# Performance work log

Hardware: AMD Instinct MI355X
Metric: run time of the kernel (lower is better)

Reference implementation:

```python
import jax, jax.numpy as jnp
import numpy as np

B = 65536          # graphs (agents)
NODES_PER = 9      # 1 torso + 8 joints
N = B * NODES_PER
D = 64
SOFTPLUS_BIAS = float(np.log(np.expm1(1.0)))  # biased_softplus_1.0 from NormalParamExtractor


def _star_edges():
    # bidirectional torso<->joint star per 9-node graph
    base = np.arange(B, dtype=np.int64) * NODES_PER          # torso ids [B]
    torso = np.repeat(base, 8)                               # [8B]
    joint = (base[:, None] + np.arange(1, 9, dtype=np.int64)[None, :]).reshape(-1)  # [8B]
    src = np.concatenate([torso, joint])                     # torso->joint, joint->torso
    dst = np.concatenate([joint, torso])
    return jnp.asarray(np.stack([src, dst], axis=0))         # [2, 16B]


def setup_inputs() -> dict:
    key = jax.random.key(0)
    ks = jax.random.split(key, 12)
    s = lambda fan_in: 1.0 / np.sqrt(fan_in)
    inp = {
        "x": jax.random.normal(ks[0], (N, 11), dtype=jnp.float32),
        "edge_index": _star_edges(),
        # input projections
        "W_joint": jax.random.uniform(ks[1], (2, D), jnp.float32, -s(2), s(2)),
        "b_joint": jnp.zeros((D,), jnp.float32),
        "W_torso": jax.random.uniform(ks[2], (11, D), jnp.float32, -s(11), s(11)),
        "b_torso": jnp.zeros((D,), jnp.float32),
        # GraphConv 1: lin_rel (bias) on aggregated neighbors + lin_root (no bias)
        "W_rel1": jax.random.uniform(ks[3], (D, D), jnp.float32, -s(D), s(D)),
        "b_rel1": jnp.zeros((D,), jnp.float32),
        "W_root1": jax.random.uniform(ks[4], (D, D), jnp.float32, -s(D), s(D)),
        # GraphConv 2
        "W_rel2": jax.random.uniform(ks[5], (D, D), jnp.float32, -s(D), s(D)),
        "b_rel2": jnp.zeros((D,), jnp.float32),
        "W_root2": jax.random.uniform(ks[6], (D, D), jnp.float32, -s(D), s(D)),
        # 8 per-joint heads Linear(64, 2)
        "W_heads": jax.random.uniform(ks[7], (8, D, 2), jnp.float32, -s(D), s(D)),
        "b_heads": jnp.zeros((8, 2), jnp.float32),
    }
    return inp


def _graph_conv(h, src, dst, W_rel, b_rel, W_root, n):
    # GraphConv (aggr='add'): out[i] = lin_rel(sum_{j->i} h[j]) + lin_root(h[i])
    agg = jax.ops.segment_sum(h[src], dst, num_segments=n)   # [N, D]
    return agg @ W_rel + b_rel + h @ W_root


def reference(x, edge_index, W_joint, b_joint, W_torso, b_torso,
              W_rel1, b_rel1, W_root1, W_rel2, b_rel2, W_root2,
              W_heads, b_heads):
    n = x.shape[0]
    b = n // NODES_PER
    xg = x.reshape(b, NODES_PER, 11)
    h_torso = xg[:, :1, :] @ W_torso + b_torso              # [b, 1, D]  (node 0 of each graph)
    h_joint = xg[:, 1:, :2] @ W_joint + b_joint             # [b, 8, D]
    h = jnp.concatenate([h_torso, h_joint], axis=1).reshape(n, D)
    src, dst = edge_index[0], edge_index[1]
    h = jnp.tanh(_graph_conv(h, src, dst, W_rel1, b_rel1, W_root1, n))
    h = jnp.tanh(_graph_conv(h, src, dst, W_rel2, b_rel2, W_root2, n))
    joints = h.reshape(b, NODES_PER, D)[:, 1:, :]           # [b, 8, D]
    out = jnp.einsum('bjd,jdo->bjo', joints, W_heads) + b_heads  # [b, 8, 2]
    loc = out[..., 0]                                       # [b, 8]
    scale = jax.nn.softplus(out[..., 1] + SOFTPLUS_BIAS)    # biased_softplus_1.0
    return loc, scale
```

## Files before the change

kernel.cpp:

```cpp
#include <hip/hip_runtime.h>


typedef __attribute__((ext_vector_type(8))) short bf16x8;
typedef __attribute__((ext_vector_type(4))) float f32x4;

#define SOFTPLUS_BIAS 0.5413248546129181f

#define LDS_H   0
#define LDS_S   18432
#define LDS_SZ  20480

__device__ __forceinline__ unsigned int cvtpk(float lo, float hi) {
  unsigned int r;
  asm("v_cvt_pk_bf16_f32 %0, %1, %2" : "=v"(r) : "v"(lo), "v"(hi));
  return r;
}
__device__ __forceinline__ float asf(unsigned int u) {
  union { unsigned int i; float f; } v; v.i = u; return v.f;
}
__device__ __forceinline__ unsigned short f2bf(float f) {
  union { float f; unsigned int i; } v; v.f = f;
  unsigned int lsb = (v.i >> 16) & 1u;
  return (unsigned short)((v.i + 0x7fffu + lsb) >> 16);
}
__device__ __forceinline__ float fast_tanh(float x) {
  float e = __expf(2.0f * x);
  return 1.0f - 2.0f * __builtin_amdgcn_rcpf(e + 1.0f);
}

__global__ void pack_weights(const float* __restrict__ Wrel1, const float* __restrict__ Wroot1,
                             const float* __restrict__ Wrel2, const float* __restrict__ Wroot2,
                             const float* __restrict__ Wheads, unsigned short* __restrict__ ws) {
  int id = blockIdx.x * 256 + threadIdx.x;
  if (id < 16384) {
    const float* W = (id < 4096) ? Wrel1 : (id < 8192) ? Wroot1 : (id < 12288) ? Wrel2 : Wroot2;
    int m = id & 4095;
    int e = m & 7, lane = (m >> 3) & 63, nt = (m >> 9) & 3, ks = m >> 11;
    int k = ((lane >> 4) << 3) + e + (ks << 5);
    int col = (nt << 4) + (lane & 15);
    ws[id] = f2bf(W[k * 64 + col]);
  } else if (id < 17408) {
    int m = id - 16384;
    int e = m & 7, lane = (m >> 3) & 63, ks = m >> 9;
    int k = ((lane >> 4) << 3) + e + (ks << 5);
    int c = lane & 15, j = c >> 1, o = c & 1;
    ws[id] = f2bf(Wheads[(j * 64 + k) * 2 + o]);
  }
}

__launch_bounds__(256, 5)
__global__ void actor_main(const float* __restrict__ x,
                           const float* __restrict__ Wj_g, const float* __restrict__ bj_g,
                           const float* __restrict__ Wt_g, const float* __restrict__ bt_g,
                           const float* __restrict__ brel1_g, const float* __restrict__ brel2_g,
                           const float* __restrict__ bh_g,
                           const unsigned short* __restrict__ wsw,
                           float* __restrict__ out) {
  __shared__ __align__(16) unsigned char smem[LDS_SZ];
  const int t = threadIdx.x;
  const int lane = t & 63;
  const int w = t >> 6;
  const int gbase = blockIdx.x << 4;
  const int l15 = lane & 15;
  const int q = lane >> 4;
  const int ks16 = q << 4;
  const int relc = l15 + (w << 4);

  const bf16x8* wsv = reinterpret_cast<const bf16x8*>(wsw);

  bf16x8 bRel0  = wsv[(0 + w) * 64 + lane];
  bf16x8 bRel1  = wsv[(4 + w) * 64 + lane];
  bf16x8 bRoot0 = wsv[512 + (0 + w) * 64 + lane];
  bf16x8 bRoot1 = wsv[512 + (4 + w) * 64 + lane];

  float Wtr[11];
#pragma unroll
  for (int k = 0; k < 11; k++) Wtr[k] = Wt_g[k * 64 + lane];
  const float btr = bt_g[lane];
  const float Wj0 = Wj_g[lane], Wj1 = Wj_g[64 + lane], bjr = bj_g[lane];
  const float brelA = brel1_g[relc], brelB = brel2_g[relc];

  unsigned int aggA[9];
#pragma unroll
  for (int m = 0; m < 9; m++) {
    int r = (m << 4) + l15;
    int g = (57 * r) >> 9;
    int node = r - 9 * g;
    int row = (node == 0) ? g : 9 * g;
    unsigned int base = (node == 0) ? (unsigned)LDS_S : 0u;
    aggA[m] = base + row * 128 + (ks16 ^ ((row & 7) << 4));
  }
  const unsigned int h0b = l15 * 128 + (unsigned)(ks16 ^ ((l15 & 7) << 4));
  unsigned int wb[4];
#pragma unroll
  for (int i = 0; i < 4; i++) {
    int rr = (q << 2) + i;
    wb[i] = rr * 128 + (unsigned)((2 * relc) ^ ((rr & 7) << 4));
  }

  const int w_u = __builtin_amdgcn_readfirstlane(w);
#pragma unroll
  for (int it = 0; it < 4; it++) {
    const int g = w_u + (it << 2);
    const float* __restrict__ xr = x + (size_t)(gbase + g) * 99;
    float acc1 = btr;
#pragma unroll
    for (int k = 0; k < 11; k++) acc1 += xr[k] * Wtr[k];
    int trow = 9 * g;
    *reinterpret_cast<unsigned short*>(smem + trow * 128 + ((2 * lane) ^ ((trow & 7) << 4))) =
        (unsigned short)cvtpk(acc1, acc1);
    float sx0 = 0.f, sx1 = 0.f;
#pragma unroll
    for (int j = 0; j < 8; j++) {
      float x0 = xr[11 + 11 * j];
      float x1 = xr[12 + 11 * j];
      sx0 += x0; sx1 += x1;
      float accj = bjr + x0 * Wj0 + x1 * Wj1;
      int row = 9 * g + 1 + j;
      *reinterpret_cast<unsigned short*>(smem + row * 128 + ((2 * lane) ^ ((row & 7) << 4))) =
          (unsigned short)cvtpk(accj, accj);
    }
    float s = 8.0f * bjr + sx0 * Wj0 + sx1 * Wj1;
    *reinterpret_cast<unsigned short*>(smem + LDS_S + g * 128 + ((2 * lane) ^ ((g & 7) << 4))) =
        (unsigned short)cvtpk(s, s);
  }
  __syncthreads();

  f32x4 acc[9];
#pragma unroll
  for (int layer = 0; layer < 2; layer++) {
    const float brel = layer ? brelB : brelA;

    if (layer == 1) {
      bRel0  = wsv[1024 + (0 + w) * 64 + lane];
      bRel1  = wsv[1024 + (4 + w) * 64 + lane];
      bRoot0 = wsv[1024 + 512 + (0 + w) * 64 + lane];
      bRoot1 = wsv[1024 + 512 + (4 + w) * 64 + lane];
      int gS = t >> 4, dq = t & 15;
      int rb = dq << 3;
      float s0 = 0.f, s1 = 0.f, s2 = 0.f, s3 = 0.f;
#pragma unroll
      for (int j = 0; j < 8; j++) {
        int row = 9 * gS + 1 + j;
        uint2 p = *reinterpret_cast<const uint2*>(smem + row * 128 + (rb ^ ((row & 7) << 4)));
        s0 += asf(p.x << 16); s1 += asf(p.x & 0xffff0000u);
        s2 += asf(p.y << 16); s3 += asf(p.y & 0xffff0000u);
      }
      uint2 o; o.x = cvtpk(s0, s1); o.y = cvtpk(s2, s3);
      *reinterpret_cast<uint2*>(smem + LDS_S + gS * 128 + (rb ^ ((gS & 7) << 4))) = o;
      __syncthreads();
    }

#pragma unroll
    for (int m = 0; m < 9; m++) {
      bf16x8 ag0 = *reinterpret_cast<const bf16x8*>(smem + aggA[m]);
      bf16x8 ag1 = *reinterpret_cast<const bf16x8*>(smem + (aggA[m] ^ 64u));
      bf16x8 a0  = *reinterpret_cast<const bf16x8*>(smem + h0b + m * 2048);
      bf16x8 a1  = *reinterpret_cast<const bf16x8*>(smem + (h0b ^ 64u) + m * 2048);
      f32x4 c = {brel, brel, brel, brel};
      c = __builtin_amdgcn_mfma_f32_16x16x32_bf16(ag0, bRel0, c, 0, 0, 0);
      c = __builtin_amdgcn_mfma_f32_16x16x32_bf16(ag1, bRel1, c, 0, 0, 0);
      c = __builtin_amdgcn_mfma_f32_16x16x32_bf16(a0, bRoot0, c, 0, 0, 0);
      acc[m] = __builtin_amdgcn_mfma_f32_16x16x32_bf16(a1, bRoot1, c, 0, 0, 0);
    }
    __syncthreads();

#pragma unroll
    for (int m = 0; m < 9; m++) {
      const int off = m * 2048;
      unsigned p0 = cvtpk(fast_tanh(acc[m][0]), fast_tanh(acc[m][1]));
      unsigned p1 = cvtpk(fast_tanh(acc[m][2]), fast_tanh(acc[m][3]));
      *reinterpret_cast<unsigned short*>(smem + wb[0] + off) = (unsigned short)p0;
      *reinterpret_cast<unsigned short*>(smem + wb[1] + off) = (unsigned short)(p0 >> 16);
      *reinterpret_cast<unsigned short*>(smem + wb[2] + off) = (unsigned short)p1;
      *reinterpret_cast<unsigned short*>(smem + wb[3] + off) = (unsigned short)(p1 >> 16);
    }
    __syncthreads();
  }

  {
    bf16x8 hb0 = wsv[2048 + lane];
    bf16x8 hb1 = wsv[2048 + 64 + lane];
    int c = l15;
#pragma unroll
    for (int u = 0; u < 2; u++) {
      int tt = (w << 1) + u;
      int jr = (tt << 4) + l15;
      int arow = 9 * (jr >> 3) + 1 + (jr & 7);
      unsigned ha = arow * 128 + (unsigned)(ks16 ^ ((arow & 7) << 4));
      bf16x8 a0 = *reinterpret_cast<const bf16x8*>(smem + ha);
      bf16x8 a1 = *reinterpret_cast<const bf16x8*>(smem + (ha ^ 64u));
      f32x4 z = {0.f, 0.f, 0.f, 0.f};
      z = __builtin_amdgcn_mfma_f32_16x16x32_bf16(a0, hb0, z, 0, 0, 0);
      z = __builtin_amdgcn_mfma_f32_16x16x32_bf16(a1, hb1, z, 0, 0, 0);
#pragma unroll
      for (int i = 0; i < 4; i++) {
        int r = (tt << 4) + (q << 2) + i;
        int gg = r >> 3, j2 = r & 7;
        if (c == 2 * j2) {
          out[(size_t)(gbase + gg) * 8 + j2] = z[i] + bh_g[2 * j2];
        } else if (c == 2 * j2 + 1) {
          float zz = z[i] + bh_g[2 * j2 + 1] + SOFTPLUS_BIAS;
          float sp = (zz > 20.0f) ? zz : __logf(1.0f + __expf(zz));
          out[524288 + (size_t)(gbase + gg) * 8 + j2] = sp;
        }
      }
    }
  }
}

extern "C" void kernel_launch(void* const* d_in, const int* in_sizes, int n_in,
                              void* d_out, int out_size, void* d_ws, size_t ws_size,
                              hipStream_t stream) {
  const float* x      = (const float*)d_in[0];
  const float* Wj     = (const float*)d_in[2];
  const float* bj     = (const float*)d_in[3];
  const float* Wt     = (const float*)d_in[4];
  const float* bt     = (const float*)d_in[5];
  const float* Wrel1  = (const float*)d_in[6];
  const float* brel1  = (const float*)d_in[7];
  const float* Wroot1 = (const float*)d_in[8];
  const float* Wrel2  = (const float*)d_in[9];
  const float* brel2  = (const float*)d_in[10];
  const float* Wroot2 = (const float*)d_in[11];
  const float* Wheads = (const float*)d_in[12];
  const float* bh     = (const float*)d_in[13];
  unsigned short* ws16 = (unsigned short*)d_ws;
  float* out = (float*)d_out;

  hipLaunchKernelGGL(pack_weights, dim3(68), dim3(256), 0, stream,
                     Wrel1, Wroot1, Wrel2, Wroot2, Wheads, ws16);
  hipLaunchKernelGGL(actor_main, dim3(4096), dim3(256), 0, stream,
                     x, Wj, bj, Wt, bt, brel1, brel2, bh, ws16, out);
}
```

Before: 63.05 us.

## Split GraphConv MFMA tiles 2x2 across waves with padded 10-row graph layout

Each wave now handles half the row tiles and two column tiles, instead of all nine row tiles and one column tile. The A fragments loaded from LDS are reused across two output column tiles, which cuts LDS reads. Graphs are padded to 10 rows so the 160 rows split evenly into 5 tiles per wave half. This increases LDS size, lowers the launch-bound occupancy from 5 to 4, and adds 10% padding compute plus more weight registers.

```diff
diff --git a/kernel.cpp b/kernel.cpp
--- a/kernel.cpp
+++ b/kernel.cpp
@@ -6,9 +6,8 @@
 
 #define SOFTPLUS_BIAS 0.5413248546129181f
 
-#define LDS_H   0
-#define LDS_S   18432
-#define LDS_SZ  20480
+#define LDS_S   20480
+#define LDS_SZ  22528
 
 __device__ __forceinline__ unsigned int cvtpk(float lo, float hi) {
   unsigned int r;
@@ -48,7 +47,7 @@
   }
 }
 
-__launch_bounds__(256, 5)
+__launch_bounds__(256, 4)
 __global__ void actor_main(const float* __restrict__ x,
                            const float* __restrict__ Wj_g, const float* __restrict__ bj_g,
                            const float* __restrict__ Wt_g, const float* __restrict__ bt_g,
@@ -60,42 +59,43 @@
   const int t = threadIdx.x;
   const int lane = t & 63;
   const int w = t >> 6;
+  const int mh = w >> 1;
+  const int nh = w & 1;
   const int gbase = blockIdx.x << 4;
   const int l15 = lane & 15;
   const int q = lane >> 4;
   const int ks16 = q << 4;
-  const int relc = l15 + (w << 4);
+  const int relc0 = l15 + (nh << 5);
+  const int relc1 = relc0 + 16;
 
   const bf16x8* wsv = reinterpret_cast<const bf16x8*>(wsw);
-
-  bf16x8 bRel0  = wsv[(0 + w) * 64 + lane];
-  bf16x8 bRel1  = wsv[(4 + w) * 64 + lane];
-  bf16x8 bRoot0 = wsv[512 + (0 + w) * 64 + lane];
-  bf16x8 bRoot1 = wsv[512 + (4 + w) * 64 + lane];
 
   float Wtr[11];
 #pragma unroll
   for (int k = 0; k < 11; k++) Wtr[k] = Wt_g[k * 64 + lane];
   const float btr = bt_g[lane];
   const float Wj0 = Wj_g[lane], Wj1 = Wj_g[64 + lane], bjr = bj_g[lane];
-  const float brelA = brel1_g[relc], brelB = brel2_g[relc];
-
-  unsigned int aggA[9];
-#pragma unroll
-  for (int m = 0; m < 9; m++) {
-    int r = (m << 4) + l15;
-    int g = (57 * r) >> 9;
-    int node = r - 9 * g;
-    int row = (node == 0) ? g : 9 * g;
-    unsigned int base = (node == 0) ? (unsigned)LDS_S : 0u;
-    aggA[m] = base + row * 128 + (ks16 ^ ((row & 7) << 4));
-  }
-  const unsigned int h0b = l15 * 128 + (unsigned)(ks16 ^ ((l15 & 7) << 4));
-  unsigned int wb[4];
+  const float brelA0 = brel1_g[relc0], brelA1 = brel1_g[relc1];
+  const float brelB0 = brel2_g[relc0], brelB1 = brel2_g[relc1];
+
+  unsigned int aggA[5];
+#pragma unroll
+  for (int mm = 0; mm < 5; mm++) {
+    int r = ((5 * mh + mm) << 4) + l15;
+    int g = (r * 205) >> 11;
+    int node = r - 10 * g;
+    if (node == 0)
+      aggA[mm] = (unsigned)(LDS_S + g * 128 + (ks16 ^ ((g & 7) << 4)));
+    else
+      aggA[mm] = (unsigned)((10 * g) * 128 + (ks16 ^ (((10 * g) & 7) << 4)));
+  }
+  const unsigned int h0bW = l15 * 128 + (unsigned)(ks16 ^ ((l15 & 7) << 4)) + mh * 10240;
+  unsigned int wb0[4], wb1[4];
 #pragma unroll
   for (int i = 0; i < 4; i++) {
     int rr = (q << 2) + i;
-    wb[i] = rr * 128 + (unsigned)((2 * relc) ^ ((rr & 7) << 4));
+    wb0[i] = rr * 128 + (unsigned)((2 * relc0) ^ ((rr & 7) << 4)) + mh * 10240;
+    wb1[i] = rr * 128 + (unsigned)((2 * relc1) ^ ((rr & 7) << 4)) + mh * 10240;
   }
 
   const int w_u = __builtin_amdgcn_readfirstlane(w);
@@ -106,7 +106,7 @@
     float acc1 = btr;
 #pragma unroll
     for (int k = 0; k < 11; k++) acc1 += xr[k] * Wtr[k];
-    int trow = 9 * g;
+    int trow = 10 * g;
     *reinterpret_cast<unsigned short*>(smem + trow * 128 + ((2 * lane) ^ ((trow & 7) << 4))) =
         (unsigned short)cvtpk(acc1, acc1);
     float sx0 = 0.f, sx1 = 0.f;
@@ -116,7 +116,7 @@
       float x1 = xr[12 + 11 * j];
       sx0 += x0; sx1 += x1;
       float accj = bjr + x0 * Wj0 + x1 * Wj1;
-      int row = 9 * g + 1 + j;
+      int row = 10 * g + 1 + j;
       *reinterpret_cast<unsigned short*>(smem + row * 128 + ((2 * lane) ^ ((row & 7) << 4))) =
           (unsigned short)cvtpk(accj, accj);
     }
@@ -126,22 +126,29 @@
   }
   __syncthreads();
 
-  f32x4 acc[9];
+  const int nt0 = nh << 1;
+  f32x4 acc[5][2];
 #pragma unroll
   for (int layer = 0; layer < 2; layer++) {
-    const float brel = layer ? brelB : brelA;
+    const int lb = layer ? 1024 : 0;
+    bf16x8 bRel00  = wsv[lb + nt0 * 64 + lane];
+    bf16x8 bRel01  = wsv[lb + 256 + nt0 * 64 + lane];
+    bf16x8 bRel10  = wsv[lb + (nt0 + 1) * 64 + lane];
+    bf16x8 bRel11  = wsv[lb + 256 + (nt0 + 1) * 64 + lane];
+    bf16x8 bRoot00 = wsv[lb + 512 + nt0 * 64 + lane];
+    bf16x8 bRoot01 = wsv[lb + 768 + nt0 * 64 + lane];
+    bf16x8 bRoot10 = wsv[lb + 512 + (nt0 + 1) * 64 + lane];
+    bf16x8 bRoot11 = wsv[lb + 768 + (nt0 + 1) * 64 + lane];
+    const float brel0 = layer ? brelB0 : brelA0;
+    const float brel1 = layer ? brelB1 : brelA1;
 
     if (layer == 1) {
-      bRel0  = wsv[1024 + (0 + w) * 64 + lane];
-      bRel1  = wsv[1024 + (4 + w) * 64 + lane];
-      bRoot0 = wsv[1024 + 512 + (0 + w) * 64 + lane];
-      bRoot1 = wsv[1024 + 512 + (4 + w) * 64 + lane];
       int gS = t >> 4, dq = t & 15;
       int rb = dq << 3;
       float s0 = 0.f, s1 = 0.f, s2 = 0.f, s3 = 0.f;
 #pragma unroll
       for (int j = 0; j < 8; j++) {
-        int row = 9 * gS + 1 + j;
+        int row = 10 * gS + 1 + j;
         uint2 p = *reinterpret_cast<const uint2*>(smem + row * 128 + (rb ^ ((row & 7) << 4)));
         s0 += asf(p.x << 16); s1 += asf(p.x & 0xffff0000u);
         s2 += asf(p.y << 16); s3 += asf(p.y & 0xffff0000u);
@@ -152,28 +159,39 @@
     }
 
 #pragma unroll
-    for (int m = 0; m < 9; m++) {
-      bf16x8 ag0 = *reinterpret_cast<const bf16x8*>(smem + aggA[m]);
-      bf16x8 ag1 = *reinterpret_cast<const bf16x8*>(smem + (aggA[m] ^ 64u));
-      bf16x8 a0  = *reinterpret_cast<const bf16x8*>(smem + h0b + m * 2048);
-      bf16x8 a1  = *reinterpret_cast<const bf16x8*>(smem + (h0b ^ 64u) + m * 2048);
-      f32x4 c = {brel, brel, brel, brel};
-      c = __builtin_amdgcn_mfma_f32_16x16x32_bf16(ag0, bRel0, c, 0, 0, 0);
-      c = __builtin_amdgcn_mfma_f32_16x16x32_bf16(ag1, bRel1, c, 0, 0, 0);
-      c = __builtin_amdgcn_mfma_f32_16x16x32_bf16(a0, bRoot0, c, 0, 0, 0);
-      acc[m] = __builtin_amdgcn_mfma_f32_16x16x32_bf16(a1, bRoot1, c, 0, 0, 0);
+    for (int mm = 0; mm < 5; mm++) {
+      bf16x8 ag0 = *reinterpret_cast<const bf16x8*>(smem + aggA[mm]);
+      bf16x8 ag1 = *reinterpret_cast<const bf16x8*>(smem + (aggA[mm] ^ 64u));
+      bf16x8 a0  = *reinterpret_cast<const bf16x8*>(smem + h0bW + mm * 2048);
+      bf16x8 a1  = *reinterpret_cast<const bf16x8*>(smem + ((h0bW + mm * 2048) ^ 64u));
+      f32x4 c0 = {brel0, brel0, brel0, brel0};
+      c0 = __builtin_amdgcn_mfma_f32_16x16x32_bf16(ag0, bRel00, c0, 0, 0, 0);
+      c0 = __builtin_amdgcn_mfma_f32_16x16x32_bf16(ag1, bRel01, c0, 0, 0, 0);
+      c0 = __builtin_amdgcn_mfma_f32_16x16x32_bf16(a0, bRoot00, c0, 0, 0, 0);
+      acc[mm][0] = __builtin_amdgcn_mfma_f32_16x16x32_bf16(a1, bRoot01, c0, 0, 0, 0);
+      f32x4 c1 = {brel1, brel1, brel1, brel1};
+      c1 = __builtin_amdgcn_mfma_f32_16x16x32_bf16(ag0, bRel10, c1, 0, 0, 0);
+      c1 = __builtin_amdgcn_mfma_f32_16x16x32_bf16(ag1, bRel11, c1, 0, 0, 0);
+      c1 = __builtin_amdgcn_mfma_f32_16x16x32_bf16(a0, bRoot10, c1, 0, 0, 0);
+      acc[mm][1] = __builtin_amdgcn_mfma_f32_16x16x32_bf16(a1, bRoot11, c1, 0, 0, 0);
     }
     __syncthreads();
 
 #pragma unroll
-    for (int m = 0; m < 9; m++) {
-      const int off = m * 2048;
-      unsigned p0 = cvtpk(fast_tanh(acc[m][0]), fast_tanh(acc[m][1]));
-      unsigned p1 = cvtpk(fast_tanh(acc[m][2]), fast_tanh(acc[m][3]));
-      *reinterpret_cast<unsigned short*>(smem + wb[0] + off) = (unsigned short)p0;
-      *reinterpret_cast<unsigned short*>(smem + wb[1] + off) = (unsigned short)(p0 >> 16);
-      *reinterpret_cast<unsigned short*>(smem + wb[2] + off) = (unsigned short)p1;
-      *reinterpret_cast<unsigned short*>(smem + wb[3] + off) = (unsigned short)(p1 >> 16);
+    for (int mm = 0; mm < 5; mm++) {
+      const int off = mm * 2048;
+      unsigned p0 = cvtpk(fast_tanh(acc[mm][0][0]), fast_tanh(acc[mm][0][1]));
+      unsigned p1 = cvtpk(fast_tanh(acc[mm][0][2]), fast_tanh(acc[mm][0][3]));
+      *reinterpret_cast<unsigned short*>(smem + wb0[0] + off) = (unsigned short)p0;
+      *reinterpret_cast<unsigned short*>(smem + wb0[1] + off) = (unsigned short)(p0 >> 16);
+      *reinterpret_cast<unsigned short*>(smem + wb0[2] + off) = (unsigned short)p1;
+      *reinterpret_cast<unsigned short*>(smem + wb0[3] + off) = (unsigned short)(p1 >> 16);
+      unsigned p2 = cvtpk(fast_tanh(acc[mm][1][0]), fast_tanh(acc[mm][1][1]));
+      unsigned p3 = cvtpk(fast_tanh(acc[mm][1][2]), fast_tanh(acc[mm][1][3]));
+      *reinterpret_cast<unsigned short*>(smem + wb1[0] + off) = (unsigned short)p2;
+      *reinterpret_cast<unsigned short*>(smem + wb1[1] + off) = (unsigned short)(p2 >> 16);
+      *reinterpret_cast<unsigned short*>(smem + wb1[2] + off) = (unsigned short)p3;
+      *reinterpret_cast<unsigned short*>(smem + wb1[3] + off) = (unsigned short)(p3 >> 16);
     }
     __syncthreads();
   }
@@ -186,7 +204,7 @@
     for (int u = 0; u < 2; u++) {
       int tt = (w << 1) + u;
       int jr = (tt << 4) + l15;
-      int arow = 9 * (jr >> 3) + 1 + (jr & 7);
+      int arow = 10 * (jr >> 3) + 1 + (jr & 7);
       unsigned ha = arow * 128 + (unsigned)(ks16 ^ ((arow & 7) << 4));
       bf16x8 a0 = *reinterpret_cast<const bf16x8*>(smem + ha);
       bf16x8 a1 = *reinterpret_cast<const bf16x8*>(smem + (ha ^ 64u));
```

Result: slower. 70.13 us (+11.2%).

## Make each wave own four graphs to drop block-wide barriers

Applied to the files above, without the earlier changes.

Each wavefront now owns its own four graphs, kept in a private LDS region padded to 12 rows per graph. Each wave computes all 64 output columns over 3 M-tiles, so __syncthreads is replaced by compiler fences. Weights are reloaded per layer from global memory rather than held in registers. The per-wave accumulator grows to 12 tiles, so launch bounds drop from 5 to 3 blocks per CU, trading occupancy for removing cross-wave synchronisation. Padding to 12 rows also wastes a quarter of the MFMA rows.

```diff
diff --git a/kernel.cpp b/kernel.cpp
--- a/kernel.cpp
+++ b/kernel.cpp
@@ -5,10 +5,9 @@
 typedef __attribute__((ext_vector_type(4))) float f32x4;
 
 #define SOFTPLUS_BIAS 0.5413248546129181f
-
-#define LDS_H   0
-#define LDS_S   18432
-#define LDS_SZ  20480
+#define LDS_SB  24576
+#define LDS_SZ  26624
+#define FENCE() asm volatile("" ::: "memory")
 
 __device__ __forceinline__ unsigned int cvtpk(float lo, float hi) {
   unsigned int r;
@@ -48,7 +47,7 @@
   }
 }
 
-__launch_bounds__(256, 5)
+__launch_bounds__(256, 3)
 __global__ void actor_main(const float* __restrict__ x,
                            const float* __restrict__ Wj_g, const float* __restrict__ bj_g,
                            const float* __restrict__ Wt_g, const float* __restrict__ bt_g,
@@ -64,50 +63,45 @@
   const int l15 = lane & 15;
   const int q = lane >> 4;
   const int ks16 = q << 4;
-  const int relc = l15 + (w << 4);
+  const unsigned HB = (unsigned)(w * 6144);
+  const unsigned SB = (unsigned)(LDS_SB + w * 512);
 
   const bf16x8* wsv = reinterpret_cast<const bf16x8*>(wsw);
-
-  bf16x8 bRel0  = wsv[(0 + w) * 64 + lane];
-  bf16x8 bRel1  = wsv[(4 + w) * 64 + lane];
-  bf16x8 bRoot0 = wsv[512 + (0 + w) * 64 + lane];
-  bf16x8 bRoot1 = wsv[512 + (4 + w) * 64 + lane];
 
   float Wtr[11];
 #pragma unroll
   for (int k = 0; k < 11; k++) Wtr[k] = Wt_g[k * 64 + lane];
   const float btr = bt_g[lane];
   const float Wj0 = Wj_g[lane], Wj1 = Wj_g[64 + lane], bjr = bj_g[lane];
-  const float brelA = brel1_g[relc], brelB = brel2_g[relc];
-
-  unsigned int aggA[9];
-#pragma unroll
-  for (int m = 0; m < 9; m++) {
-    int r = (m << 4) + l15;
-    int g = (57 * r) >> 9;
-    int node = r - 9 * g;
-    int row = (node == 0) ? g : 9 * g;
-    unsigned int base = (node == 0) ? (unsigned)LDS_S : 0u;
-    aggA[m] = base + row * 128 + (ks16 ^ ((row & 7) << 4));
-  }
-  const unsigned int h0b = l15 * 128 + (unsigned)(ks16 ^ ((l15 & 7) << 4));
-  unsigned int wb[4];
-#pragma unroll
-  for (int i = 0; i < 4; i++) {
-    int rr = (q << 2) + i;
-    wb[i] = rr * 128 + (unsigned)((2 * relc) ^ ((rr & 7) << 4));
-  }
+  float brelA[4], brelB[4];
+#pragma unroll
+  for (int nt = 0; nt < 4; nt++) {
+    brelA[nt] = brel1_g[l15 + (nt << 4)];
+    brelB[nt] = brel2_g[l15 + (nt << 4)];
+  }
+
+  unsigned aggA[3];
+#pragma unroll
+  for (int mt = 0; mt < 3; mt++) {
+    int r = (mt << 4) + l15;
+    int g = (r * 43) >> 9;
+    int node = r - 12 * g;
+    int trow = 12 * g;
+    aggA[mt] = (node == 0)
+        ? (SB + g * 128 + (unsigned)(ks16 ^ (g << 4)))
+        : (HB + trow * 128 + (unsigned)(ks16 ^ ((trow & 7) << 4)));
+  }
+  const unsigned h0b = HB + l15 * 128 + (unsigned)(ks16 ^ ((l15 & 7) << 4));
 
   const int w_u = __builtin_amdgcn_readfirstlane(w);
 #pragma unroll
   for (int it = 0; it < 4; it++) {
-    const int g = w_u + (it << 2);
-    const float* __restrict__ xr = x + (size_t)(gbase + g) * 99;
+    const float* __restrict__ xr = x + (size_t)(gbase + (w_u << 2) + it) * 99;
     float acc1 = btr;
 #pragma unroll
     for (int k = 0; k < 11; k++) acc1 += xr[k] * Wtr[k];
-    int trow = 9 * g;
-    *reinterpret_cast<unsigned short*>(smem + trow * 128 + ((2 * lane) ^ ((trow & 7) << 4))) =
+    int trow = 12 * it;
+    *reinterpret_cast<unsigned short*>(smem + HB + trow * 128 + ((2 * lane) ^ ((trow & 7) << 4))) =
         (unsigned short)cvtpk(acc1, acc1);
     float sx0 = 0.f, sx1 = 0.f;
 #pragma unroll
@@ -116,78 +110,100 @@
       float x1 = xr[12 + 11 * j];
       sx0 += x0; sx1 += x1;
       float accj = bjr + x0 * Wj0 + x1 * Wj1;
-      int row = 9 * g + 1 + j;
-      *reinterpret_cast<unsigned short*>(smem + row * 128 + ((2 * lane) ^ ((row & 7) << 4))) =
+      int row = 12 * it + 1 + j;
+      *reinterpret_cast<unsigned short*>(smem + HB + row * 128 + ((2 * lane) ^ ((row & 7) << 4))) =
           (unsigned short)cvtpk(accj, accj);
     }
     float s = 8.0f * bjr + sx0 * Wj0 + sx1 * Wj1;
-    *reinterpret_cast<unsigned short*>(smem + LDS_S + g * 128 + ((2 * lane) ^ ((g & 7) << 4))) =
+    *reinterpret_cast<unsigned short*>(smem + SB + it * 128 + ((2 * lane) ^ (it << 4))) =
         (unsigned short)cvtpk(s, s);
   }
-  __syncthreads();
-
-  f32x4 acc[9];
+  FENCE();
+
+  f32x4 acc[3][4];
 #pragma unroll
   for (int layer = 0; layer < 2; layer++) {
-    const float brel = layer ? brelB : brelA;
+    const int lb = layer ? 1024 : 0;
 
     if (layer == 1) {
-      bRel0  = wsv[1024 + (0 + w) * 64 + lane];
-      bRel1  = wsv[1024 + (4 + w) * 64 + lane];
-      bRoot0 = wsv[1024 + 512 + (0 + w) * 64 + lane];
-      bRoot1 = wsv[1024 + 512 + (4 + w) * 64 + lane];
-      int gS = t >> 4, dq = t & 15;
+      int gS = lane >> 4, dq = lane & 15;
       int rb = dq << 3;
       float s0 = 0.f, s1 = 0.f, s2 = 0.f, s3 = 0.f;
 #pragma unroll
       for (int j = 0; j < 8; j++) {
-        int row = 9 * gS + 1 + j;
-        uint2 p = *reinterpret_cast<const uint2*>(smem + row * 128 + (rb ^ ((row & 7) << 4)));
+        int row = 12 * gS + 1 + j;
+        uint2 p = *reinterpret_cast<const uint2*>(smem + HB + row * 128 + (rb ^ ((row & 7) << 4)));
         s0 += asf(p.x << 16); s1 += asf(p.x & 0xffff0000u);
         s2 += asf(p.y << 16); s3 += asf(p.y & 0xffff0000u);
       }
       uint2 o; o.x = cvtpk(s0, s1); o.y = cvtpk(s2, s3);
-      *reinterpret_cast<uint2*>(smem + LDS_S + gS * 128 + (rb ^ ((gS & 7) << 4))) = o;
-      __syncthreads();
-    }
-
-#pragma unroll
-    for (int m = 0; m < 9; m++) {
-      bf16x8 ag0 = *reinterpret_cast<const bf16x8*>(smem + aggA[m]);
-      bf16x8 ag1 = *reinterpret_cast<const bf16x8*>(smem + (aggA[m] ^ 64u));
-      bf16x8 a0  = *reinterpret_cast<const bf16x8*>(smem + h0b + m * 2048);
-      bf16x8 a1  = *reinterpret_cast<const bf16x8*>(smem + (h0b ^ 64u) + m * 2048);
-      f32x4 c = {brel, brel, brel, brel};
-      c = __builtin_amdgcn_mfma_f32_16x16x32_bf16(ag0, bRel0, c, 0, 0, 0);
-      c = __builtin_amdgcn_mfma_f32_16x16x32_bf16(ag1, bRel1, c, 0, 0, 0);
-      c = __builtin_amdgcn_mfma_f32_16x16x32_bf16(a0, bRoot0, c, 0, 0, 0);
-      acc[m] = __builtin_amdgcn_mfma_f32_16x16x32_bf16(a1, bRoot1, c, 0, 0, 0);
-    }
-    __syncthreads();
-
-#pragma unroll
-    for (int m = 0; m < 9; m++) {
-      const int off = m * 2048;
-      unsigned p0 = cvtpk(fast_tanh(acc[m][0]), fast_tanh(acc[m][1]));
-      unsigned p1 = cvtpk(fast_tanh(acc[m][2]), fast_tanh(acc[m][3]));
-      *reinterpret_cast<unsigned short*>(smem + wb[0] + off) = (unsigned short)p0;
-      *reinterpret_cast<unsigned short*>(smem + wb[1] + off) = (unsigned short)(p0 >> 16);
-      *reinterpret_cast<unsigned short*>(smem + wb[2] + off) = (unsigned short)p1;
-      *reinterpret_cast<unsigned short*>(smem + wb[3] + off) = (unsigned short)(p1 >> 16);
-    }
-    __syncthreads();
+      *reinterpret_cast<uint2*>(smem + SB + gS * 128 + (rb ^ (gS << 4))) = o;
+      FENCE();
+    }
+
+    bf16x8 bf[4][2];
+#pragma unroll
+    for (int nt = 0; nt < 4; nt++) {
+      bf[nt][0] = wsv[lb + nt * 64 + lane];
+      bf[nt][1] = wsv[lb + 256 + nt * 64 + lane];
+    }
+#pragma unroll
+    for (int mt = 0; mt < 3; mt++) {
+      bf16x8 ag0 = *reinterpret_cast<const bf16x8*>(smem + aggA[mt]);
+      bf16x8 ag1 = *reinterpret_cast<const bf16x8*>(smem + (aggA[mt] ^ 64u));
+#pragma unroll
+      for (int nt = 0; nt < 4; nt++) {
+        float br = layer ? brelB[nt] : brelA[nt];
+        f32x4 c = {br, br, br, br};
+        c = __builtin_amdgcn_mfma_f32_16x16x32_bf16(ag0, bf[nt][0], c, 0, 0, 0);
+        acc[mt][nt] = __builtin_amdgcn_mfma_f32_16x16x32_bf16(ag1, bf[nt][1], c, 0, 0, 0);
+      }
+    }
+#pragma unroll
+    for (int nt = 0; nt < 4; nt++) {
+      bf[nt][0] = wsv[lb + 512 + nt * 64 + lane];
+      bf[nt][1] = wsv[lb + 768 + nt * 64 + lane];
+    }
+#pragma unroll
+    for (int mt = 0; mt < 3; mt++) {
+      bf16x8 a0 = *reinterpret_cast<const bf16x8*>(smem + h0b + mt * 2048);
+      bf16x8 a1 = *reinterpret_cast<const bf16x8*>(smem + ((h0b + mt * 2048) ^ 64u));
+#pragma unroll
+      for (int nt = 0; nt < 4; nt++) {
+        f32x4 c = __builtin_amdgcn_mfma_f32_16x16x32_bf16(a0, bf[nt][0], acc[mt][nt], 0, 0, 0);
+        acc[mt][nt] = __builtin_amdgcn_mfma_f32_16x16x32_bf16(a1, bf[nt][1], c, 0, 0, 0);
+      }
+    }
+    FENCE();
+
+#pragma unroll
+    for (int mt = 0; mt < 3; mt++) {
+#pragma unroll
+      for (int nt = 0; nt < 4; nt++) {
+        unsigned p0 = cvtpk(fast_tanh(acc[mt][nt][0]), fast_tanh(acc[mt][nt][1]));
+        unsigned p1 = cvtpk(fast_tanh(acc[mt][nt][2]), fast_tanh(acc[mt][nt][3]));
+        const unsigned colp = (unsigned)((nt << 5) + 2 * l15);
+#pragma unroll
+        for (int i = 0; i < 4; i++) {
+          int rr = (mt << 4) + (q << 2) + i;
+          unsigned addr = HB + rr * 128 + (colp ^ (((q << 2) + i & 7) << 4));
+          unsigned short v = (i == 0) ? (unsigned short)p0 : (i == 1) ? (unsigned short)(p0 >> 16)
+                           : (i == 2) ? (unsigned short)p1 : (unsigned short)(p1 >> 16);
+          *reinterpret_cast<unsigned short*>(smem + addr) = v;
+        }
+      }
+    }
+    FENCE();
   }
 
   {
     bf16x8 hb0 = wsv[2048 + lane];
     bf16x8 hb1 = wsv[2048 + 64 + lane];
-    int c = l15;
 #pragma unroll
     for (int u = 0; u < 2; u++) {
-      int tt = (w << 1) + u;
-      int jr = (tt << 4) + l15;
-      int arow = 9 * (jr >> 3) + 1 + (jr & 7);
-      unsigned ha = arow * 128 + (unsigned)(ks16 ^ ((arow & 7) << 4));
+      int jw = (u << 4) + l15;
+      int arow = 12 * (jw >> 3) + 1 + (jw & 7);
+      unsigned ha = HB + arow * 128 + (unsigned)(ks16 ^ ((arow & 7) << 4));
       bf16x8 a0 = *reinterpret_cast<const bf16x8*>(smem + ha);
       bf16x8 a1 = *reinterpret_cast<const bf16x8*>(smem + (ha ^ 64u));
       f32x4 z = {0.f, 0.f, 0.f, 0.f};
@@ -195,14 +211,15 @@
       z = __builtin_amdgcn_mfma_f32_16x16x32_bf16(a1, hb1, z, 0, 0, 0);
 #pragma unroll
       for (int i = 0; i < 4; i++) {
-        int r = (tt << 4) + (q << 2) + i;
+        int r = (u << 4) + (q << 2) + i;
         int gg = r >> 3, j2 = r & 7;
-        if (c == 2 * j2) {
-          out[(size_t)(gbase + gg) * 8 + j2] = z[i] + bh_g[2 * j2];
-        } else if (c == 2 * j2 + 1) {
+        size_t G = (size_t)(gbase + (w << 2) + gg);
+        if (l15 == 2 * j2) {
+          out[G * 8 + j2] = z[i] + bh_g[2 * j2];
+        } else if (l15 == 2 * j2 + 1) {
           float zz = z[i] + bh_g[2 * j2 + 1] + SOFTPLUS_BIAS;
           float sp = (zz > 20.0f) ? zz : __logf(1.0f + __expf(zz));
-          out[524288 + (size_t)(gbase + gg) * 8 + j2] = sp;
+          out[524288 + G * 8 + j2] = sp;
         }
       }
     }
```

Result: slower. 72.27 us (+14.6%).
